# Kernel tuning notes

Hardware: AMD Instinct MI355X
Metric: run time of the kernel (lower is better)

The kernel has to match this reference:

```python
import jax, jax.numpy as jnp
import numpy as np

N = 50000   # nodes
E = 640000  # edges
IN = 256    # in_dim
H = 128     # hidden
OUT = 40    # out_dim
EPS = 1e-5  # BatchNorm eps


def setup_inputs() -> dict:
    key = jax.random.key(0)
    ks = jax.random.split(key, 14)
    x = jax.random.normal(ks[0], (N, IN), jnp.float32)
    edge_index = jax.random.randint(ks[1], (2, E), 0, N)
    def lin(k, fan_in, shape):
        return jax.random.normal(k, shape, jnp.float32) / np.float32(np.sqrt(fan_in))
    return {
        "x": x,
        "edge_index": edge_index,
        # block 0 (256 -> 128, has res_proj)
        "W0": lin(ks[2], IN, (IN, H)),
        "b0": jnp.zeros((H,), jnp.float32),
        "g0": jnp.ones((H,), jnp.float32),
        "be0": jnp.zeros((H,), jnp.float32),
        "pW": lin(ks[3], IN, (IN, H)),
        "pb": jnp.zeros((H,), jnp.float32),
        # block 1 (128 -> 128, identity residual)
        "W1": lin(ks[4], H, (H, H)),
        "b1": jnp.zeros((H,), jnp.float32),
        "g1": jnp.ones((H,), jnp.float32),
        "be1": jnp.zeros((H,), jnp.float32),
        # head
        "hW": lin(ks[5], H, (H, OUT)),
        "hb": jnp.zeros((OUT,), jnp.float32),
    }


def _gcn_conv(x, W, b, edge_index):
    """GCNConv(improved=True): x' = D^-1/2 (A + 2I) D^-1/2 (x W) + b."""
    h = x @ W  # [N, dout]
    row, col = edge_index[0], edge_index[1]  # source -> target
    # degree of A + 2I (edge_weight = 1, self-loop fill = 2.0)
    deg = jnp.zeros((N,), h.dtype).at[col].add(1.0) + 2.0
    dis = jax.lax.rsqrt(deg)  # deg > 0 always (self-loops)
    norm = dis[row] * dis[col]  # [E]
    # neighbor aggregation: scatter-add normalized messages to targets
    agg = jnp.zeros_like(h).at[col].add(norm[:, None] * h[row])
    # self-loop contribution with weight 2.0
    agg = agg + (2.0 * dis * dis)[:, None] * h
    return agg + b


def _bn(x, gamma, beta):
    # batch statistics (training-mode BatchNorm math), biased variance
    m = jnp.mean(x, axis=0)
    v = jnp.mean(jnp.square(x - m), axis=0)
    return (x - m) * jax.lax.rsqrt(v + EPS) * gamma + beta


def reference(x, edge_index, W0, b0, g0, be0, pW, pb, W1, b1, g1, be1, hW, hb):
    # block 0: conv -> bn -> relu -> (+ res_proj(x))
    out = jax.nn.relu(_bn(_gcn_conv(x, W0, b0, edge_index), g0, be0))
    x1 = out + (x @ pW + pb)
    # block 1: conv -> bn -> relu -> (+ identity)
    out = jax.nn.relu(_bn(_gcn_conv(x1, W1, b1, edge_index), g1, be1))
    x2 = out + x1
    return x2 @ hW + hb  # [N, OUT]
```

## Files before the change

kernel.cpp:

```cpp
#include <hip/hip_runtime.h>

#define H 128
#define IN_DIM 256
#define OUT_DIM 40
#define EPS 1e-5f

typedef unsigned short ushortT;
typedef __attribute__((ext_vector_type(8))) short bf16x8;
typedef __attribute__((ext_vector_type(4))) float f32x4;

static __device__ __forceinline__ ushortT f2bf(float f) {
    union { float f; unsigned u; } v; v.f = f;
    unsigned r = v.u + 0x7FFF + ((v.u >> 16) & 1);
    return (ushortT)(r >> 16);
}
static __device__ __forceinline__ unsigned pk2(float a, float b) {
    return (unsigned)f2bf(a) | ((unsigned)f2bf(b) << 16);
}
static __device__ __forceinline__ float bflo(unsigned v) {
    union { unsigned u; float f; } t; t.u = v << 16; return t.f;
}
static __device__ __forceinline__ float bfhi(unsigned v) {
    union { unsigned u; float f; } t; t.u = v & 0xFFFF0000u; return t.f;
}
static __device__ __forceinline__ float i2f(int v) {
    union { int i; float f; } t; t.i = v; return t.f;
}
static __device__ __forceinline__ int f2i(float v) {
    union { float f; int i; } t; t.f = v; return t.i;
}


__global__ __launch_bounds__(256) void count_xcd(const int* __restrict__ ei, int E, int nper,
                                                 int* __restrict__ cnt) {
    int xcd = blockIdx.x & 7;
    int nchunk = gridDim.x >> 3;
    int chunk = blockIdx.x >> 3;
    int csz = (E + nchunk - 1) / nchunk;
    int beg = chunk * csz;
    int end = min(E, beg + csz);
    for (int e = beg + (int)threadIdx.x; e < end; e += 256) {
        int c = ei[E + e];
        if (c / nper == xcd) atomicAdd(&cnt[c], 1);
    }
}

__global__ __launch_bounds__(256) void scan_block_sum(const int* __restrict__ cnt, int* __restrict__ bsum,
                                                      float* __restrict__ dis, int N) {
    __shared__ int s[256];
    int i = blockIdx.x * 256 + threadIdx.x;
    int c = (i < N) ? cnt[i] : -1;
    int v = (i < N) ? c + 1 : 0;
    if (i < N) dis[i] = rsqrtf((float)c + 2.0f);
    s[threadIdx.x] = v;
    __syncthreads();
    for (int o = 128; o > 0; o >>= 1) {
        if (threadIdx.x < o) s[threadIdx.x] += s[threadIdx.x + o];
        __syncthreads();
    }
    if (threadIdx.x == 0) bsum[blockIdx.x] = s[0];
}

__global__ void scan_tops(const int* __restrict__ bsum, int* __restrict__ boff, int* __restrict__ rowptrN, int nb) {
    __shared__ int s[256];
    int t = threadIdx.x;
    int v = (t < nb) ? bsum[t] : 0;
    s[t] = v;
    __syncthreads();
    for (int o = 1; o < 256; o <<= 1) {
        int u = (t >= o) ? s[t - o] : 0;
        __syncthreads();
        s[t] += u;
        __syncthreads();
    }
    if (t < nb) boff[t] = s[t] - v;
    if (t == 255) *rowptrN = s[255];
}

__global__ __launch_bounds__(256) void scan_final(const int* __restrict__ cnt, const int* __restrict__ boff,
                                                  const float* __restrict__ dis,
                                                  int* __restrict__ rowptr, int* __restrict__ cursor,
                                                  int2* __restrict__ recs, int N) {
    __shared__ int s[256];
    int t = threadIdx.x;
    int i = blockIdx.x * 256 + t;
    int v = (i < N) ? cnt[i] + 1 : 0;
    s[t] = v;
    __syncthreads();
    for (int o = 1; o < 256; o <<= 1) {
        int u = (t >= o) ? s[t - o] : 0;
        __syncthreads();
        s[t] += u;
        __syncthreads();
    }
    if (i < N) {
        int e = boff[blockIdx.x] + s[t] - v;
        rowptr[i] = e;
        cursor[i] = e + 1;
        float d = dis[i];
        int2 r; r.x = i; r.y = f2i(2.0f * d * d);
        recs[e] = r;
    }
}

__global__ __launch_bounds__(256) void fill_xcd(const int* __restrict__ ei, int E, int nper,
                                                const float* __restrict__ dis,
                                                int* __restrict__ cursor, int2* __restrict__ recs) {
    int xcd = blockIdx.x & 7;
    int nchunk = gridDim.x >> 3;
    int chunk = blockIdx.x >> 3;
    int csz = (E + nchunk - 1) / nchunk;
    int beg = chunk * csz;
    int end = min(E, beg + csz);
    for (int e = beg + (int)threadIdx.x; e < end; e += 256) {
        int c = ei[E + e];
        if (c / nper == xcd) {
            int r = ei[e];
            int slot = atomicAdd(&cursor[c], 1);
            int2 rec; rec.x = r; rec.y = f2i(dis[r] * dis[c]);
            recs[slot] = rec;
        }
    }
}


__global__ __launch_bounds__(256) void prep_weights(const float* __restrict__ W0, const float* __restrict__ pW,
                                                    const float* __restrict__ W1, const float* __restrict__ hW,
                                                    ushortT* __restrict__ Wt0, ushortT* __restrict__ WtP,
                                                    ushortT* __restrict__ Wt1, ushortT* __restrict__ WtH,
                                                    int* __restrict__ cnt, float* __restrict__ stats, int N) {
    int i = blockIdx.x * 256 + threadIdx.x;
    if (i < 32768) { int n = i >> 8, k = i & 255; Wt0[i] = f2bf(W0[k * 128 + n]); WtP[i] = f2bf(pW[k * 128 + n]); }
    if (i < 16384) { int n = i >> 7, k = i & 127; Wt1[i] = f2bf(W1[k * 128 + n]); }
    if (i < 6144)  { int n = i >> 7, k = i & 127; WtH[i] = (n < OUT_DIM) ? f2bf(hW[k * OUT_DIM + n]) : (ushortT)0; }
    if (i < N) cnt[i] = 0;
    if (i < 512) stats[i] = 0.f;
}


static __device__ __forceinline__ void g0_loads(const float* __restrict__ X, int brow, int kc,
                                                int tid, int N, float4 pf[4]) {
#pragma unroll
    for (int i = 0; i < 4; ++i) {
        int idx = i * 512 + tid;
        int row = idx >> 5, c4 = idx & 31;
        int gr = brow + row;
        pf[i] = make_float4(0.f, 0.f, 0.f, 0.f);
        if (gr < N) pf[i] = *(const float4*)&X[(size_t)gr * IN_DIM + kc * 128 + c4 * 4];
    }
}
static __device__ __forceinline__ void g0_write(ushortT* __restrict__ Sbuf, int tid, const float4 pf[4]) {
#pragma unroll
    for (int i = 0; i < 4; ++i) {
        int idx = i * 512 + tid;
        int row = idx >> 5, c4 = idx & 31;
        uint2 p;
        p.x = pk2(pf[i].x, pf[i].y);
        p.y = pk2(pf[i].z, pf[i].w);
        *(uint2*)&Sbuf[row * 136 + c4 * 4] = p;
    }
}

__global__ __launch_bounds__(512) void mgemm0d(const float* __restrict__ X,
                                               const ushortT* __restrict__ Wt0,
                                               const ushortT* __restrict__ WtP,
                                               const float* __restrict__ pb,
                                               ushortT* __restrict__ Oh,
                                               ushortT* __restrict__ Op,
                                               int N) {
    __shared__ __align__(16) ushortT S2[2][64 * 136];
    int tid = threadIdx.x;
    int brow = blockIdx.x * 64;
    int w = tid >> 6, lane = tid & 63;
    int lm = lane & 15, lk = lane >> 4;
    int mat = w >> 2;
    int colbase = (w & 3) * 32;
    const ushortT* Wt = mat ? WtP : Wt0;

    bf16x8 breg[2][8];
#pragma unroll
    for (int nt = 0; nt < 2; ++nt)
#pragma unroll
        for (int kk = 0; kk < 8; ++kk)
            breg[nt][kk] = *(const bf16x8*)&Wt[(size_t)(colbase + nt * 16 + lm) * IN_DIM + kk * 32 + lk * 8];
    float bb[2];
    bb[0] = mat ? pb[colbase + lm] : 0.f;
    bb[1] = mat ? pb[colbase + 16 + lm] : 0.f;

    float4 pf[4];
    g0_loads(X, brow, 0, tid, N, pf);
    g0_write(S2[0], tid, pf);
    __syncthreads();
    g0_loads(X, brow, 1, tid, N, pf);

    f32x4 acc[4][2];
#pragma unroll
    for (int mt = 0; mt < 4; ++mt)
#pragma unroll
        for (int nt = 0; nt < 2; ++nt) acc[mt][nt] = (f32x4)0.f;

#pragma unroll
    for (int kk = 0; kk < 4; ++kk) {
        bf16x8 af[4];
#pragma unroll
        for (int mt = 0; mt < 4; ++mt)
            af[mt] = *(const bf16x8*)&S2[0][(mt * 16 + lm) * 136 + kk * 32 + lk * 8];
#pragma unroll
        for (int nt = 0; nt < 2; ++nt)
#pragma unroll
            for (int mt = 0; mt < 4; ++mt)
                acc[mt][nt] = __builtin_amdgcn_mfma_f32_16x16x32_bf16(af[mt], breg[nt][kk], acc[mt][nt], 0, 0, 0);
    }
    g0_write(S2[1], tid, pf);
    __syncthreads();
#pragma unroll
    for (int kk = 0; kk < 4; ++kk) {
        bf16x8 af[4];
#pragma unroll
        for (int mt = 0; mt < 4; ++mt)
            af[mt] = *(const bf16x8*)&S2[1][(mt * 16 + lm) * 136 + kk * 32 + lk * 8];
#pragma unroll
        for (int nt = 0; nt < 2; ++nt)
#pragma unroll
            for (int mt = 0; mt < 4; ++mt)
                acc[mt][nt] = __builtin_amdgcn_mfma_f32_16x16x32_bf16(af[mt], breg[nt][4 + kk], acc[mt][nt], 0, 0, 0);
    }
    __syncthreads();
#pragma unroll
    for (int mt = 0; mt < 4; ++mt)
#pragma unroll
        for (int nt = 0; nt < 2; ++nt) {
            int col = colbase + nt * 16 + lm;
#pragma unroll
            for (int j = 0; j < 4; ++j) {
                int row = mt * 16 + lk * 4 + j;
                S2[mat][row * 136 + col] = f2bf(acc[mt][nt][j] + bb[nt]);
            }
        }
    __syncthreads();
#pragma unroll
    for (int i = 0; i < 4; ++i) {
        int idx = i * 512 + tid;
        int m2 = idx >> 10;
        int rem = idx & 1023;
        int row = rem >> 4, colq = rem & 15;
        int gr = brow + row;
        if (gr < N) {
            uint4 v = *(const uint4*)&S2[m2][row * 136 + colq * 8];
            ushortT* O = m2 ? Op : Oh;
            *(uint4*)&O[(size_t)gr * 128 + colq * 8] = v;
        }
    }
}


__global__ __launch_bounds__(512) void mgemm1_fused(const uint4* __restrict__ aggb,
                                                    const uint4* __restrict__ projb,
                                                    const float* __restrict__ stats,
                                                    const float* __restrict__ g,
                                                    const float* __restrict__ be,
                                                    const ushortT* __restrict__ Wt1,
                                                    ushortT* __restrict__ O,
                                                    uint4* __restrict__ x1b,
                                                    int N) {
    __shared__ __align__(16) ushortT S[17408];
    __shared__ float sc[128], sh[128];
    int tid = threadIdx.x;
    int brow = blockIdx.x * 128;

    if (tid < 128) {
        float mean = stats[tid] / (float)N;
        float var = stats[128 + tid] / (float)N - mean * mean;
        float inv = rsqrtf(var + EPS);
        float s = g[tid] * inv;
        sc[tid] = s;
        sh[tid] = be[tid] - mean * s;
    }
    __syncthreads();

#pragma unroll
    for (int i = 0; i < 4; ++i) {
        int idx = i * 512 + tid;
        int row = idx >> 4, q = idx & 15;
        int gr = brow + row;
        uint4 a = make_uint4(0u, 0u, 0u, 0u), p = a;
        if (gr < N) {
            size_t gidx = (size_t)gr * 16 + q;
            a = aggb[gidx];
            p = projb[gidx];
        }
        int ch = q * 8;
        float v0 = fmaxf(fmaf(bflo(a.x), sc[ch + 0], sh[ch + 0]), 0.f) + bflo(p.x);
        float v1 = fmaxf(fmaf(bfhi(a.x), sc[ch + 1], sh[ch + 1]), 0.f) + bfhi(p.x);
        float v2 = fmaxf(fmaf(bflo(a.y), sc[ch + 2], sh[ch + 2]), 0.f) + bflo(p.y);
        float v3 = fmaxf(fmaf(bfhi(a.y), sc[ch + 3], sh[ch + 3]), 0.f) + bfhi(p.y);
        float v4 = fmaxf(fmaf(bflo(a.z), sc[ch + 4], sh[ch + 4]), 0.f) + bflo(p.z);
        float v5 = fmaxf(fmaf(bfhi(a.z), sc[ch + 5], sh[ch + 5]), 0.f) + bfhi(p.z);
        float v6 = fmaxf(fmaf(bflo(a.w), sc[ch + 6], sh[ch + 6]), 0.f) + bflo(p.w);
        float v7 = fmaxf(fmaf(bfhi(a.w), sc[ch + 7], sh[ch + 7]), 0.f) + bfhi(p.w);
        uint4 pv;
        pv.x = pk2(v0, v1);
        pv.y = pk2(v2, v3);
        pv.z = pk2(v4, v5);
        pv.w = pk2(v6, v7);
        *(uint4*)&S[row * 136 + q * 8] = pv;
        if (gr < N) x1b[(size_t)gr * 16 + q] = pv;
    }
    __syncthreads();

    int w = tid >> 6, lane = tid & 63;
    int lm = lane & 15, lk = lane >> 4;
    int rh = (w >> 2) * 64;
    int colbase = (w & 3) * 32;

    bf16x8 breg[2][4];
#pragma unroll
    for (int nt = 0; nt < 2; ++nt)
#pragma unroll
        for (int ks = 0; ks < 4; ++ks)
            breg[nt][ks] = *(const bf16x8*)&Wt1[(size_t)(colbase + nt * 16 + lm) * H + ks * 32 + lk * 8];

    f32x4 acc[4][2];
#pragma unroll
    for (int mt = 0; mt < 4; ++mt)
#pragma unroll
        for (int nt = 0; nt < 2; ++nt) acc[mt][nt] = (f32x4)0.f;

#pragma unroll
    for (int ks = 0; ks < 4; ++ks) {
        bf16x8 af[4];
#pragma unroll
        for (int mt = 0; mt < 4; ++mt)
            af[mt] = *(const bf16x8*)&S[(rh + mt * 16 + lm) * 136 + ks * 32 + lk * 8];
#pragma unroll
        for (int nt = 0; nt < 2; ++nt)
#pragma unroll
            for (int mt = 0; mt < 4; ++mt)
                acc[mt][nt] = __builtin_amdgcn_mfma_f32_16x16x32_bf16(af[mt], breg[nt][ks], acc[mt][nt], 0, 0, 0);
    }

    __syncthreads();
#pragma unroll
    for (int mt = 0; mt < 4; ++mt)
#pragma unroll
        for (int nt = 0; nt < 2; ++nt) {
            int col = colbase + nt * 16 + lm;
#pragma unroll
            for (int j = 0; j < 4; ++j) {
                int row = rh + mt * 16 + lk * 4 + j;
                S[row * 136 + col] = f2bf(acc[mt][nt][j]);
            }
        }
    __syncthreads();
#pragma unroll
    for (int i = 0; i < 4; ++i) {
        int idx = i * 512 + tid;
        int row = idx >> 4, colq = idx & 15;
        int gr = brow + row;
        if (gr < N) {
            uint4 v = *(const uint4*)&S[row * 136 + colq * 8];
            *(uint4*)&O[(size_t)gr * 128 + colq * 8] = v;
        }
    }
}


__global__ __launch_bounds__(256) void aggregate_rec(const ushortT* __restrict__ h,
                                                     const int* __restrict__ rowptr,
                                                     const int2* __restrict__ recs,
                                                     ushortT* __restrict__ aggb, int N) {
    int n = blockIdx.x * 4 + (threadIdx.x >> 6);
    if (n >= N) return;
    int lane = threadIdx.x & 63;
    int half = lane >> 5, cl = lane & 31;
    int beg = rowptr[n], end = rowptr[n + 1];
    const uint2* h2 = (const uint2*)h;
    float a0 = 0.f, a1 = 0.f, a2 = 0.f, a3 = 0.f;
    float b0 = 0.f, b1 = 0.f, b2 = 0.f, b3 = 0.f;
    int idx = beg + half;
    for (; idx + 2 < end; idx += 4) {
        int2 r0 = recs[idx];
        int2 r1 = recs[idx + 2];
        uint2 v0 = h2[(size_t)r0.x * 32 + cl];
        uint2 v1 = h2[(size_t)r1.x * 32 + cl];
        float n0 = i2f(r0.y), n1 = i2f(r1.y);
        a0 = fmaf(n0, bflo(v0.x), a0); a1 = fmaf(n0, bfhi(v0.x), a1);
        a2 = fmaf(n0, bflo(v0.y), a2); a3 = fmaf(n0, bfhi(v0.y), a3);
        b0 = fmaf(n1, bflo(v1.x), b0); b1 = fmaf(n1, bfhi(v1.x), b1);
        b2 = fmaf(n1, bflo(v1.y), b2); b3 = fmaf(n1, bfhi(v1.y), b3);
    }
    if (idx < end) {
        int2 r0 = recs[idx];
        uint2 v0 = h2[(size_t)r0.x * 32 + cl];
        float n0 = i2f(r0.y);
        a0 = fmaf(n0, bflo(v0.x), a0); a1 = fmaf(n0, bfhi(v0.x), a1);
        a2 = fmaf(n0, bflo(v0.y), a2); a3 = fmaf(n0, bfhi(v0.y), a3);
    }
    a0 += b0; a1 += b1; a2 += b2; a3 += b3;
    a0 += __shfl_xor(a0, 32);
    a1 += __shfl_xor(a1, 32);
    a2 += __shfl_xor(a2, 32);
    a3 += __shfl_xor(a3, 32);
    if (half == 0) {
        uint2 o;
        o.x = pk2(a0, a1);
        o.y = pk2(a2, a3);
        ((uint2*)aggb)[(size_t)n * 32 + cl] = o;
    }
}


__global__ __launch_bounds__(256) void stats_bf(const unsigned* __restrict__ v, int totalU,
                                                float* __restrict__ sums) {
    int tid = blockIdx.x * 256 + threadIdx.x;
    int stride = gridDim.x * 256;
    float sx = 0.f, sy = 0.f, qx = 0.f, qy = 0.f;
    for (int i = tid; i < totalU; i += stride) {
        unsigned u = v[i];
        float a = bflo(u), b = bfhi(u);
        sx += a; sy += b;
        qx = fmaf(a, a, qx); qy = fmaf(b, b, qy);
    }
    __shared__ float l0[256], l1[256], l2[256], l3[256];
    int t = threadIdx.x;
    l0[t] = sx; l1[t] = sy; l2[t] = qx; l3[t] = qy;
    __syncthreads();
    if (t < 64) {
        sx = (l0[t] + l0[t + 64]) + (l0[t + 128] + l0[t + 192]);
        sy = (l1[t] + l1[t + 64]) + (l1[t + 128] + l1[t + 192]);
        qx = (l2[t] + l2[t + 64]) + (l2[t + 128] + l2[t + 192]);
        qy = (l3[t] + l3[t + 64]) + (l3[t + 128] + l3[t + 192]);
        atomicAdd(&sums[2 * t], sx);
        atomicAdd(&sums[2 * t + 1], sy);
        atomicAdd(&sums[128 + 2 * t], qx);
        atomicAdd(&sums[128 + 2 * t + 1], qy);
    }
}


__global__ __launch_bounds__(256) void head_fused(const uint4* __restrict__ aggb,
                                                  const uint4* __restrict__ x1b,
                                                  const float* __restrict__ stats,
                                                  const float* __restrict__ g,
                                                  const float* __restrict__ be,
                                                  const ushortT* __restrict__ WtH,
                                                  const float* __restrict__ hb,
                                                  float* __restrict__ out, int N) {
    __shared__ __align__(16) ushortT As[64][136];
    __shared__ __align__(16) ushortT Bs[48][136];
    __shared__ float sc[128], sh[128];

    int tid = threadIdx.x;
    int brow = blockIdx.x * 64;
    int w = tid >> 6, lane = tid & 63;
    int lm = lane & 15, lk = lane >> 4;

    if (tid < 128) {
        float mean = stats[tid] / (float)N;
        float var = stats[128 + tid] / (float)N - mean * mean;
        float inv = rsqrtf(var + EPS);
        float s = g[tid] * inv;
        sc[tid] = s;
        sh[tid] = be[tid] - mean * s;
    }
    if (tid < 192) {
        int row = tid >> 2, q = tid & 3;
        const uint4* src = (const uint4*)&WtH[(size_t)row * H + q * 32];
        uint4 a = src[0], b = src[1], c = src[2], d = src[3];
        uint4* dst = (uint4*)&Bs[row][q * 32];
        dst[0] = a; dst[1] = b; dst[2] = c; dst[3] = d;
    }
    __syncthreads();
#pragma unroll
    for (int k = 0; k < 4; ++k) {
        int idx = k * 256 + tid;
        int row = idx >> 4, colq = idx & 15;
        int gr = brow + row;
        uint4 a = make_uint4(0u, 0u, 0u, 0u), x = a;
        if (gr < N) {
            size_t gidx = (size_t)brow * 16 + idx;
            a = aggb[gidx];
            x = x1b[gidx];
        }
        int ch = colq * 8;
        float v0 = fmaxf(fmaf(bflo(a.x), sc[ch + 0], sh[ch + 0]), 0.f) + bflo(x.x);
        float v1 = fmaxf(fmaf(bfhi(a.x), sc[ch + 1], sh[ch + 1]), 0.f) + bfhi(x.x);
        float v2 = fmaxf(fmaf(bflo(a.y), sc[ch + 2], sh[ch + 2]), 0.f) + bflo(x.y);
        float v3 = fmaxf(fmaf(bfhi(a.y), sc[ch + 3], sh[ch + 3]), 0.f) + bfhi(x.y);
        float v4 = fmaxf(fmaf(bflo(a.z), sc[ch + 4], sh[ch + 4]), 0.f) + bflo(x.z);
        float v5 = fmaxf(fmaf(bfhi(a.z), sc[ch + 5], sh[ch + 5]), 0.f) + bfhi(x.z);
        float v6 = fmaxf(fmaf(bflo(a.w), sc[ch + 6], sh[ch + 6]), 0.f) + bflo(x.w);
        float v7 = fmaxf(fmaf(bfhi(a.w), sc[ch + 7], sh[ch + 7]), 0.f) + bfhi(x.w);
        uint4 pv;
        pv.x = pk2(v0, v1);
        pv.y = pk2(v2, v3);
        pv.z = pk2(v4, v5);
        pv.w = pk2(v6, v7);
        *(uint4*)&As[row][colq * 8] = pv;
    }
    __syncthreads();

    f32x4 acc[3];
#pragma unroll
    for (int nt = 0; nt < 3; ++nt) acc[nt] = (f32x4)0.f;
#pragma unroll
    for (int ks = 0; ks < 4; ++ks) {
        bf16x8 a = *(const bf16x8*)&As[w * 16 + lm][ks * 32 + lk * 8];
#pragma unroll
        for (int nt = 0; nt < 3; ++nt) {
            bf16x8 b = *(const bf16x8*)&Bs[nt * 16 + lm][ks * 32 + lk * 8];
            acc[nt] = __builtin_amdgcn_mfma_f32_16x16x32_bf16(a, b, acc[nt], 0, 0, 0);
        }
    }
#pragma unroll
    for (int nt = 0; nt < 3; ++nt) {
        int col = nt * 16 + lm;
        if (col < OUT_DIM) {
            float bbv = hb[col];
#pragma unroll
            for (int j = 0; j < 4; ++j) {
                int r = brow + w * 16 + lk * 4 + j;
                if (r < N) out[(size_t)r * OUT_DIM + col] = acc[nt][j] + bbv;
            }
        }
    }
}


extern "C" void kernel_launch(void* const* d_in, const int* in_sizes, int n_in,
                              void* d_out, int out_size, void* d_ws, size_t ws_size,
                              hipStream_t stream) {
    const float* x   = (const float*)d_in[0];
    const int*   ei  = (const int*)d_in[1];
    const float* W0  = (const float*)d_in[2];
    const float* g0  = (const float*)d_in[4];
    const float* be0 = (const float*)d_in[5];
    const float* pW  = (const float*)d_in[6];
    const float* pb  = (const float*)d_in[7];
    const float* W1  = (const float*)d_in[8];
    const float* g1  = (const float*)d_in[10];
    const float* be1 = (const float*)d_in[11];
    const float* hW  = (const float*)d_in[12];
    const float* hb  = (const float*)d_in[13];
    float* out = (float*)d_out;

    int N = in_sizes[0] / IN_DIM;
    int E = in_sizes[1] / 2;
    size_t NH = (size_t)N * H;

    ushortT* hb16   = (ushortT*)d_ws;
    ushortT* aggb   = hb16 + NH;
    ushortT* projb  = aggb + NH;
    ushortT* x1b    = projb + NH;
    float*   dis    = (float*)(x1b + NH);
    int*     cnt    = (int*)(dis + N);
    int*     rowptr = cnt + N;
    int*     cursor = rowptr + (N + 1);
    int2*    recs   = (int2*)(cursor + N);
    float*   stats  = (float*)(recs + (E + N));
    ushortT* Wt0    = (ushortT*)(stats + 512);
    ushortT* WtP    = Wt0 + 128 * 256;
    ushortT* Wt1    = WtP + 128 * 256;
    ushortT* WtH    = Wt1 + 128 * 128;
    int*     bsum   = (int*)(WtH + 48 * 128);
    int*     boff   = bsum + 256;
    float*   stats0 = stats;
    float*   stats1 = stats + 256;

    int nb = (N + 255) / 256;
    int g64 = (N + 63) / 64;
    int g128 = (N + 127) / 128;
    int gAgg = (N + 3) / 4;

    prep_weights<<<196, 256, 0, stream>>>(W0, pW, W1, hW, Wt0, WtP, Wt1, WtH, cnt, stats, N);
    count_xcd<<<2048, 256, 0, stream>>>(ei, E, (N + 7) / 8, cnt);
    scan_block_sum<<<nb, 256, 0, stream>>>(cnt, bsum, dis, N);
    scan_tops<<<1, 256, 0, stream>>>(bsum, boff, &rowptr[N], nb);
    scan_final<<<nb, 256, 0, stream>>>(cnt, boff, dis, rowptr, cursor, recs, N);
    fill_xcd<<<2048, 256, 0, stream>>>(ei, E, (N + 7) / 8, dis, cursor, recs);

    mgemm0d<<<g64, 512, 0, stream>>>(x, Wt0, WtP, pb, hb16, projb, N);
    aggregate_rec<<<gAgg, 256, 0, stream>>>(hb16, rowptr, recs, aggb, N);
    stats_bf<<<256, 256, 0, stream>>>((const unsigned*)aggb, (int)(NH / 2), stats0);

    mgemm1_fused<<<g128, 512, 0, stream>>>((const uint4*)aggb, (const uint4*)projb, stats0, g0, be0,
                                           Wt1, hb16, (uint4*)x1b, N);
    aggregate_rec<<<gAgg, 256, 0, stream>>>(hb16, rowptr, recs, aggb, N);
    stats_bf<<<256, 256, 0, stream>>>((const unsigned*)aggb, (int)(NH / 2), stats1);

    head_fused<<<g64, 256, 0, stream>>>((const uint4*)aggb, (const uint4*)x1b, stats1, g1, be1,
                                        WtH, hb, out, N);
}
```

Measured before the change: 251.7 us.

## Fuse degree counting into first GEMM launch and unroll aggregation by four

The degree-count kernel is merged into the first GEMM launch as extra blocks after the GEMM blocks, so the edge counting runs alongside the independent X·W0/X·pW GEMM instead of as a separate serialized launch. The GEMM is moved ahead of the CSR scan and fill steps. The aggregate kernel now handles four edges per half-wave per iteration with four accumulator sets instead of two, giving more memory-level parallelism on the gathers. The cost is more registers in aggregation, and count blocks that share the 512-thread launch configuration and LDS allocation with the GEMM blocks.

```diff
diff --git a/kernel.cpp b/kernel.cpp
--- a/kernel.cpp
+++ b/kernel.cpp
@@ -31,19 +31,153 @@
 }
 
 
-__global__ __launch_bounds__(256) void count_xcd(const int* __restrict__ ei, int E, int nper,
-                                                 int* __restrict__ cnt) {
-    int xcd = blockIdx.x & 7;
-    int nchunk = gridDim.x >> 3;
-    int chunk = blockIdx.x >> 3;
-    int csz = (E + nchunk - 1) / nchunk;
-    int beg = chunk * csz;
-    int end = min(E, beg + csz);
-    for (int e = beg + (int)threadIdx.x; e < end; e += 256) {
-        int c = ei[E + e];
-        if (c / nper == xcd) atomicAdd(&cnt[c], 1);
-    }
-}
+__global__ __launch_bounds__(256) void prep_weights(const float* __restrict__ W0, const float* __restrict__ pW,
+                                                    const float* __restrict__ W1, const float* __restrict__ hW,
+                                                    ushortT* __restrict__ Wt0, ushortT* __restrict__ WtP,
+                                                    ushortT* __restrict__ Wt1, ushortT* __restrict__ WtH,
+                                                    int* __restrict__ cnt, float* __restrict__ stats, int N) {
+    int i = blockIdx.x * 256 + threadIdx.x;
+    if (i < 32768) { int n = i >> 8, k = i & 255; Wt0[i] = f2bf(W0[k * 128 + n]); WtP[i] = f2bf(pW[k * 128 + n]); }
+    if (i < 16384) { int n = i >> 7, k = i & 127; Wt1[i] = f2bf(W1[k * 128 + n]); }
+    if (i < 6144)  { int n = i >> 7, k = i & 127; WtH[i] = (n < OUT_DIM) ? f2bf(hW[k * OUT_DIM + n]) : (ushortT)0; }
+    if (i < N) cnt[i] = 0;
+    if (i < 512) stats[i] = 0.f;
+}
+
+
+static __device__ __forceinline__ void g0_loads(const float* __restrict__ X, int brow, int kc,
+                                                int tid, int N, float4 pf[4]) {
+#pragma unroll
+    for (int i = 0; i < 4; ++i) {
+        int idx = i * 512 + tid;
+        int row = idx >> 5, c4 = idx & 31;
+        int gr = brow + row;
+        pf[i] = make_float4(0.f, 0.f, 0.f, 0.f);
+        if (gr < N) pf[i] = *(const float4*)&X[(size_t)gr * IN_DIM + kc * 128 + c4 * 4];
+    }
+}
+static __device__ __forceinline__ void g0_write(ushortT* __restrict__ Sbuf, int tid, const float4 pf[4]) {
+#pragma unroll
+    for (int i = 0; i < 4; ++i) {
+        int idx = i * 512 + tid;
+        int row = idx >> 5, c4 = idx & 31;
+        uint2 p;
+        p.x = pk2(pf[i].x, pf[i].y);
+        p.y = pk2(pf[i].z, pf[i].w);
+        *(uint2*)&Sbuf[row * 136 + c4 * 4] = p;
+    }
+}
+
+__global__ __launch_bounds__(512) void gemm0_count(const float* __restrict__ X,
+                                                   const ushortT* __restrict__ Wt0,
+                                                   const ushortT* __restrict__ WtP,
+                                                   const float* __restrict__ pb,
+                                                   ushortT* __restrict__ Oh,
+                                                   ushortT* __restrict__ Op,
+                                                   const int* __restrict__ ei,
+                                                   int* __restrict__ cnt,
+                                                   int N, int E, int nper, int gemmBlocks) {
+    __shared__ __align__(16) ushortT S2[2][64 * 136];
+    int tid = threadIdx.x;
+
+    if (blockIdx.x >= gemmBlocks) {
+        int cbid = blockIdx.x - gemmBlocks;
+        int xcd = cbid & 7;
+        int nchunk = (gridDim.x - gemmBlocks) >> 3;
+        int chunk = cbid >> 3;
+        int csz = (E + nchunk - 1) / nchunk;
+        int beg = chunk * csz;
+        int end = min(E, beg + csz);
+        for (int e = beg + tid; e < end; e += 512) {
+            int c = ei[E + e];
+            if (c / nper == xcd) atomicAdd(&cnt[c], 1);
+        }
+        return;
+    }
+
+    int brow = blockIdx.x * 64;
+    int w = tid >> 6, lane = tid & 63;
+    int lm = lane & 15, lk = lane >> 4;
+    int mat = w >> 2;
+    int colbase = (w & 3) * 32;
+    const ushortT* Wt = mat ? WtP : Wt0;
+
+    bf16x8 breg[2][8];
+#pragma unroll
+    for (int nt = 0; nt < 2; ++nt)
+#pragma unroll
+        for (int kk = 0; kk < 8; ++kk)
+            breg[nt][kk] = *(const bf16x8*)&Wt[(size_t)(colbase + nt * 16 + lm) * IN_DIM + kk * 32 + lk * 8];
+    float bb[2];
+    bb[0] = mat ? pb[colbase + lm] : 0.f;
+    bb[1] = mat ? pb[colbase + 16 + lm] : 0.f;
+
+    float4 pf[4];
+    g0_loads(X, brow, 0, tid, N, pf);
+    g0_write(S2[0], tid, pf);
+    __syncthreads();
+    g0_loads(X, brow, 1, tid, N, pf);
+
+    f32x4 acc[4][2];
+#pragma unroll
+    for (int mt = 0; mt < 4; ++mt)
+#pragma unroll
+        for (int nt = 0; nt < 2; ++nt) acc[mt][nt] = (f32x4)0.f;
+
+#pragma unroll
+    for (int kk = 0; kk < 4; ++kk) {
+        bf16x8 af[4];
+#pragma unroll
+        for (int mt = 0; mt < 4; ++mt)
+            af[mt] = *(const bf16x8*)&S2[0][(mt * 16 + lm) * 136 + kk * 32 + lk * 8];
+#pragma unroll
+        for (int nt = 0; nt < 2; ++nt)
+#pragma unroll
+            for (int mt = 0; mt < 4; ++mt)
+                acc[mt][nt] = __builtin_amdgcn_mfma_f32_16x16x32_bf16(af[mt], breg[nt][kk], acc[mt][nt], 0, 0, 0);
+    }
+    g0_write(S2[1], tid, pf);
+    __syncthreads();
+#pragma unroll
+    for (int kk = 0; kk < 4; ++kk) {
+        bf16x8 af[4];
+#pragma unroll
+        for (int mt = 0; mt < 4; ++mt)
+            af[mt] = *(const bf16x8*)&S2[1][(mt * 16 + lm) * 136 + kk * 32 + lk * 8];
+#pragma unroll
+        for (int nt = 0; nt < 2; ++nt)
+#pragma unroll
+            for (int mt = 0; mt < 4; ++mt)
+                acc[mt][nt] = __builtin_amdgcn_mfma_f32_16x16x32_bf16(af[mt], breg[nt][4 + kk], acc[mt][nt], 0, 0, 0);
+    }
+    __syncthreads();
+#pragma unroll
+    for (int mt = 0; mt < 4; ++mt)
+#pragma unroll
+        for (int nt = 0; nt < 2; ++nt) {
+            int col = colbase + nt * 16 + lm;
+#pragma unroll
+            for (int j = 0; j < 4; ++j) {
+                int row = mt * 16 + lk * 4 + j;
+                S2[mat][row * 136 + col] = f2bf(acc[mt][nt][j] + bb[nt]);
+            }
+        }
+    __syncthreads();
+#pragma unroll
+    for (int i = 0; i < 4; ++i) {
+        int idx = i * 512 + tid;
+        int m2 = idx >> 10;
+        int rem = idx & 1023;
+        int row = rem >> 4, colq = rem & 15;
+        int gr = brow + row;
+        if (gr < N) {
+            uint4 v = *(const uint4*)&S2[m2][row * 136 + colq * 8];
+            ushortT* O = m2 ? Op : Oh;
+            *(uint4*)&O[(size_t)gr * 128 + colq * 8] = v;
+        }
+    }
+}
+
 
 __global__ __launch_bounds__(256) void scan_block_sum(const int* __restrict__ cnt, int* __restrict__ bsum,
                                                       float* __restrict__ dis, int N) {
@@ -124,132 +258,88 @@
 }
 
 
-__global__ __launch_bounds__(256) void prep_weights(const float* __restrict__ W0, const float* __restrict__ pW,
-                                                    const float* __restrict__ W1, const float* __restrict__ hW,
-                                                    ushortT* __restrict__ Wt0, ushortT* __restrict__ WtP,
-                                                    ushortT* __restrict__ Wt1, ushortT* __restrict__ WtH,
-                                                    int* __restrict__ cnt, float* __restrict__ stats, int N) {
-    int i = blockIdx.x * 256 + threadIdx.x;
-    if (i < 32768) { int n = i >> 8, k = i & 255; Wt0[i] = f2bf(W0[k * 128 + n]); WtP[i] = f2bf(pW[k * 128 + n]); }
-    if (i < 16384) { int n = i >> 7, k = i & 127; Wt1[i] = f2bf(W1[k * 128 + n]); }
-    if (i < 6144)  { int n = i >> 7, k = i & 127; WtH[i] = (n < OUT_DIM) ? f2bf(hW[k * OUT_DIM + n]) : (ushortT)0; }
-    if (i < N) cnt[i] = 0;
-    if (i < 512) stats[i] = 0.f;
-}
-
-
-static __device__ __forceinline__ void g0_loads(const float* __restrict__ X, int brow, int kc,
-                                                int tid, int N, float4 pf[4]) {
-#pragma unroll
-    for (int i = 0; i < 4; ++i) {
-        int idx = i * 512 + tid;
-        int row = idx >> 5, c4 = idx & 31;
-        int gr = brow + row;
-        pf[i] = make_float4(0.f, 0.f, 0.f, 0.f);
-        if (gr < N) pf[i] = *(const float4*)&X[(size_t)gr * IN_DIM + kc * 128 + c4 * 4];
-    }
-}
-static __device__ __forceinline__ void g0_write(ushortT* __restrict__ Sbuf, int tid, const float4 pf[4]) {
-#pragma unroll
-    for (int i = 0; i < 4; ++i) {
-        int idx = i * 512 + tid;
-        int row = idx >> 5, c4 = idx & 31;
-        uint2 p;
-        p.x = pk2(pf[i].x, pf[i].y);
-        p.y = pk2(pf[i].z, pf[i].w);
-        *(uint2*)&Sbuf[row * 136 + c4 * 4] = p;
-    }
-}
-
-__global__ __launch_bounds__(512) void mgemm0d(const float* __restrict__ X,
-                                               const ushortT* __restrict__ Wt0,
-                                               const ushortT* __restrict__ WtP,
-                                               const float* __restrict__ pb,
-                                               ushortT* __restrict__ Oh,
-                                               ushortT* __restrict__ Op,
-                                               int N) {
-    __shared__ __align__(16) ushortT S2[2][64 * 136];
-    int tid = threadIdx.x;
-    int brow = blockIdx.x * 64;
-    int w = tid >> 6, lane = tid & 63;
-    int lm = lane & 15, lk = lane >> 4;
-    int mat = w >> 2;
-    int colbase = (w & 3) * 32;
-    const ushortT* Wt = mat ? WtP : Wt0;
-
-    bf16x8 breg[2][8];
-#pragma unroll
-    for (int nt = 0; nt < 2; ++nt)
-#pragma unroll
-        for (int kk = 0; kk < 8; ++kk)
-            breg[nt][kk] = *(const bf16x8*)&Wt[(size_t)(colbase + nt * 16 + lm) * IN_DIM + kk * 32 + lk * 8];
-    float bb[2];
-    bb[0] = mat ? pb[colbase + lm] : 0.f;
-    bb[1] = mat ? pb[colbase + 16 + lm] : 0.f;
-
-    float4 pf[4];
-    g0_loads(X, brow, 0, tid, N, pf);
-    g0_write(S2[0], tid, pf);
-    __syncthreads();
-    g0_loads(X, brow, 1, tid, N, pf);
-
-    f32x4 acc[4][2];
-#pragma unroll
-    for (int mt = 0; mt < 4; ++mt)
-#pragma unroll
-        for (int nt = 0; nt < 2; ++nt) acc[mt][nt] = (f32x4)0.f;
-
-#pragma unroll
-    for (int kk = 0; kk < 4; ++kk) {
-        bf16x8 af[4];
-#pragma unroll
-        for (int mt = 0; mt < 4; ++mt)
-            af[mt] = *(const bf16x8*)&S2[0][(mt * 16 + lm) * 136 + kk * 32 + lk * 8];
-#pragma unroll
-        for (int nt = 0; nt < 2; ++nt)
-#pragma unroll
-            for (int mt = 0; mt < 4; ++mt)
-                acc[mt][nt] = __builtin_amdgcn_mfma_f32_16x16x32_bf16(af[mt], breg[nt][kk], acc[mt][nt], 0, 0, 0);
-    }
-    g0_write(S2[1], tid, pf);
-    __syncthreads();
-#pragma unroll
-    for (int kk = 0; kk < 4; ++kk) {
-        bf16x8 af[4];
-#pragma unroll
-        for (int mt = 0; mt < 4; ++mt)
-            af[mt] = *(const bf16x8*)&S2[1][(mt * 16 + lm) * 136 + kk * 32 + lk * 8];
-#pragma unroll
-        for (int nt = 0; nt < 2; ++nt)
-#pragma unroll
-            for (int mt = 0; mt < 4; ++mt)
-                acc[mt][nt] = __builtin_amdgcn_mfma_f32_16x16x32_bf16(af[mt], breg[nt][4 + kk], acc[mt][nt], 0, 0, 0);
-    }
-    __syncthreads();
-#pragma unroll
-    for (int mt = 0; mt < 4; ++mt)
-#pragma unroll
-        for (int nt = 0; nt < 2; ++nt) {
-            int col = colbase + nt * 16 + lm;
-#pragma unroll
-            for (int j = 0; j < 4; ++j) {
-                int row = mt * 16 + lk * 4 + j;
-                S2[mat][row * 136 + col] = f2bf(acc[mt][nt][j] + bb[nt]);
-            }
-        }
-    __syncthreads();
-#pragma unroll
-    for (int i = 0; i < 4; ++i) {
-        int idx = i * 512 + tid;
-        int m2 = idx >> 10;
-        int rem = idx & 1023;
-        int row = rem >> 4, colq = rem & 15;
-        int gr = brow + row;
-        if (gr < N) {
-            uint4 v = *(const uint4*)&S2[m2][row * 136 + colq * 8];
-            ushortT* O = m2 ? Op : Oh;
-            *(uint4*)&O[(size_t)gr * 128 + colq * 8] = v;
-        }
+__global__ __launch_bounds__(256) void aggregate_rec(const ushortT* __restrict__ h,
+                                                     const int* __restrict__ rowptr,
+                                                     const int2* __restrict__ recs,
+                                                     ushortT* __restrict__ aggb, int N) {
+    int n = blockIdx.x * 4 + (threadIdx.x >> 6);
+    if (n >= N) return;
+    int lane = threadIdx.x & 63;
+    int half = lane >> 5, cl = lane & 31;
+    int beg = rowptr[n], end = rowptr[n + 1];
+    const uint2* h2 = (const uint2*)h;
+    float a0 = 0.f, a1 = 0.f, a2 = 0.f, a3 = 0.f;
+    float b0 = 0.f, b1 = 0.f, b2 = 0.f, b3 = 0.f;
+    float c0 = 0.f, c1 = 0.f, c2 = 0.f, c3 = 0.f;
+    float d0 = 0.f, d1 = 0.f, d2 = 0.f, d3 = 0.f;
+    int idx = beg + half;
+    for (; idx + 6 < end; idx += 8) {
+        int2 r0 = recs[idx];
+        int2 r1 = recs[idx + 2];
+        int2 r2 = recs[idx + 4];
+        int2 r3 = recs[idx + 6];
+        uint2 v0 = h2[(size_t)r0.x * 32 + cl];
+        uint2 v1 = h2[(size_t)r1.x * 32 + cl];
+        uint2 v2 = h2[(size_t)r2.x * 32 + cl];
+        uint2 v3 = h2[(size_t)r3.x * 32 + cl];
+        float n0 = i2f(r0.y), n1 = i2f(r1.y), n2 = i2f(r2.y), n3 = i2f(r3.y);
+        a0 = fmaf(n0, bflo(v0.x), a0); a1 = fmaf(n0, bfhi(v0.x), a1);
+        a2 = fmaf(n0, bflo(v0.y), a2); a3 = fmaf(n0, bfhi(v0.y), a3);
+        b0 = fmaf(n1, bflo(v1.x), b0); b1 = fmaf(n1, bfhi(v1.x), b1);
+        b2 = fmaf(n1, bflo(v1.y), b2); b3 = fmaf(n1, bfhi(v1.y), b3);
+        c0 = fmaf(n2, bflo(v2.x), c0); c1 = fmaf(n2, bfhi(v2.x), c1);
+        c2 = fmaf(n2, bflo(v2.y), c2); c3 = fmaf(n2, bfhi(v2.y), c3);
+        d0 = fmaf(n3, bflo(v3.x), d0); d1 = fmaf(n3, bfhi(v3.x), d1);
+        d2 = fmaf(n3, bflo(v3.y), d2); d3 = fmaf(n3, bfhi(v3.y), d3);
+    }
+    for (; idx < end; idx += 2) {
+        int2 r0 = recs[idx];
+        uint2 v0 = h2[(size_t)r0.x * 32 + cl];
+        float n0 = i2f(r0.y);
+        a0 = fmaf(n0, bflo(v0.x), a0); a1 = fmaf(n0, bfhi(v0.x), a1);
+        a2 = fmaf(n0, bflo(v0.y), a2); a3 = fmaf(n0, bfhi(v0.y), a3);
+    }
+    a0 = (a0 + b0) + (c0 + d0);
+    a1 = (a1 + b1) + (c1 + d1);
+    a2 = (a2 + b2) + (c2 + d2);
+    a3 = (a3 + b3) + (c3 + d3);
+    a0 += __shfl_xor(a0, 32);
+    a1 += __shfl_xor(a1, 32);
+    a2 += __shfl_xor(a2, 32);
+    a3 += __shfl_xor(a3, 32);
+    if (half == 0) {
+        uint2 o;
+        o.x = pk2(a0, a1);
+        o.y = pk2(a2, a3);
+        ((uint2*)aggb)[(size_t)n * 32 + cl] = o;
+    }
+}
+
+
+__global__ __launch_bounds__(256) void stats_bf(const unsigned* __restrict__ v, int totalU,
+                                                float* __restrict__ sums) {
+    int tid = blockIdx.x * 256 + threadIdx.x;
+    int stride = gridDim.x * 256;
+    float sx = 0.f, sy = 0.f, qx = 0.f, qy = 0.f;
+    for (int i = tid; i < totalU; i += stride) {
+        unsigned u = v[i];
+        float a = bflo(u), b = bfhi(u);
+        sx += a; sy += b;
+        qx = fmaf(a, a, qx); qy = fmaf(b, b, qy);
+    }
+    __shared__ float l0[256], l1[256], l2[256], l3[256];
+    int t = threadIdx.x;
+    l0[t] = sx; l1[t] = sy; l2[t] = qx; l3[t] = qy;
+    __syncthreads();
+    if (t < 64) {
+        sx = (l0[t] + l0[t + 64]) + (l0[t + 128] + l0[t + 192]);
+        sy = (l1[t] + l1[t + 64]) + (l1[t + 128] + l1[t + 192]);
+        qx = (l2[t] + l2[t + 64]) + (l2[t + 128] + l2[t + 192]);
+        qy = (l3[t] + l3[t + 64]) + (l3[t + 128] + l3[t + 192]);
+        atomicAdd(&sums[2 * t], sx);
+        atomicAdd(&sums[2 * t + 1], sy);
+        atomicAdd(&sums[128 + 2 * t], qx);
+        atomicAdd(&sums[128 + 2 * t + 1], qy);
     }
 }
 
@@ -361,79 +451,6 @@
             uint4 v = *(const uint4*)&S[row * 136 + colq * 8];
             *(uint4*)&O[(size_t)gr * 128 + colq * 8] = v;
         }
-    }
-}
-
-
-__global__ __launch_bounds__(256) void aggregate_rec(const ushortT* __restrict__ h,
-                                                     const int* __restrict__ rowptr,
-                                                     const int2* __restrict__ recs,
-                                                     ushortT* __restrict__ aggb, int N) {
-    int n = blockIdx.x * 4 + (threadIdx.x >> 6);
-    if (n >= N) return;
-    int lane = threadIdx.x & 63;
-    int half = lane >> 5, cl = lane & 31;
-    int beg = rowptr[n], end = rowptr[n + 1];
-    const uint2* h2 = (const uint2*)h;
-    float a0 = 0.f, a1 = 0.f, a2 = 0.f, a3 = 0.f;
-    float b0 = 0.f, b1 = 0.f, b2 = 0.f, b3 = 0.f;
-    int idx = beg + half;
-    for (; idx + 2 < end; idx += 4) {
-        int2 r0 = recs[idx];
-        int2 r1 = recs[idx + 2];
-        uint2 v0 = h2[(size_t)r0.x * 32 + cl];
-        uint2 v1 = h2[(size_t)r1.x * 32 + cl];
-        float n0 = i2f(r0.y), n1 = i2f(r1.y);
-        a0 = fmaf(n0, bflo(v0.x), a0); a1 = fmaf(n0, bfhi(v0.x), a1);
-        a2 = fmaf(n0, bflo(v0.y), a2); a3 = fmaf(n0, bfhi(v0.y), a3);
-        b0 = fmaf(n1, bflo(v1.x), b0); b1 = fmaf(n1, bfhi(v1.x), b1);
-        b2 = fmaf(n1, bflo(v1.y), b2); b3 = fmaf(n1, bfhi(v1.y), b3);
-    }
-    if (idx < end) {
-        int2 r0 = recs[idx];
-        uint2 v0 = h2[(size_t)r0.x * 32 + cl];
-        float n0 = i2f(r0.y);
-        a0 = fmaf(n0, bflo(v0.x), a0); a1 = fmaf(n0, bfhi(v0.x), a1);
-        a2 = fmaf(n0, bflo(v0.y), a2); a3 = fmaf(n0, bfhi(v0.y), a3);
-    }
-    a0 += b0; a1 += b1; a2 += b2; a3 += b3;
-    a0 += __shfl_xor(a0, 32);
-    a1 += __shfl_xor(a1, 32);
-    a2 += __shfl_xor(a2, 32);
-    a3 += __shfl_xor(a3, 32);
-    if (half == 0) {
-        uint2 o;
-        o.x = pk2(a0, a1);
-        o.y = pk2(a2, a3);
-        ((uint2*)aggb)[(size_t)n * 32 + cl] = o;
-    }
-}
-
-
-__global__ __launch_bounds__(256) void stats_bf(const unsigned* __restrict__ v, int totalU,
-                                                float* __restrict__ sums) {
-    int tid = blockIdx.x * 256 + threadIdx.x;
-    int stride = gridDim.x * 256;
-    float sx = 0.f, sy = 0.f, qx = 0.f, qy = 0.f;
-    for (int i = tid; i < totalU; i += stride) {
-        unsigned u = v[i];
-        float a = bflo(u), b = bfhi(u);
-        sx += a; sy += b;
-        qx = fmaf(a, a, qx); qy = fmaf(b, b, qy);
-    }
-    __shared__ float l0[256], l1[256], l2[256], l3[256];
-    int t = threadIdx.x;
-    l0[t] = sx; l1[t] = sy; l2[t] = qx; l3[t] = qy;
-    __syncthreads();
-    if (t < 64) {
-        sx = (l0[t] + l0[t + 64]) + (l0[t + 128] + l0[t + 192]);
-        sy = (l1[t] + l1[t + 64]) + (l1[t + 128] + l1[t + 192]);
-        qx = (l2[t] + l2[t + 64]) + (l2[t + 128] + l2[t + 192]);
-        qy = (l3[t] + l3[t + 64]) + (l3[t + 128] + l3[t + 192]);
-        atomicAdd(&sums[2 * t], sx);
-        atomicAdd(&sums[2 * t + 1], sy);
-        atomicAdd(&sums[128 + 2 * t], qx);
-        atomicAdd(&sums[128 + 2 * t + 1], qy);
     }
 }
 
@@ -571,15 +588,19 @@
     int g64 = (N + 63) / 64;
     int g128 = (N + 127) / 128;
     int gAgg = (N + 3) / 4;
+    int nper = (N + 7) / 8;
+    const int CNT_BLOCKS = 1024;
 
     prep_weights<<<196, 256, 0, stream>>>(W0, pW, W1, hW, Wt0, WtP, Wt1, WtH, cnt, stats, N);
-    count_xcd<<<2048, 256, 0, stream>>>(ei, E, (N + 7) / 8, cnt);
+
+    gemm0_count<<<g64 + CNT_BLOCKS, 512, 0, stream>>>(x, Wt0, WtP, pb, hb16, projb,
+                                                      ei, cnt, N, E, nper, g64);
+
     scan_block_sum<<<nb, 256, 0, stream>>>(cnt, bsum, dis, N);
     scan_tops<<<1, 256, 0, stream>>>(bsum, boff, &rowptr[N], nb);
     scan_final<<<nb, 256, 0, stream>>>(cnt, boff, dis, rowptr, cursor, recs, N);
-    fill_xcd<<<2048, 256, 0, stream>>>(ei, E, (N + 7) / 8, dis, cursor, recs);
-
-    mgemm0d<<<g64, 512, 0, stream>>>(x, Wt0, WtP, pb, hb16, projb, N);
+    fill_xcd<<<2048, 256, 0, stream>>>(ei, E, nper, dis, cursor, recs);
+
     aggregate_rec<<<gAgg, 256, 0, stream>>>(hb16, rowptr, recs, aggb, N);
     stats_bf<<<256, 256, 0, stream>>>((const unsigned*)aggb, (int)(NH / 2), stats0);
 
```

Result: faster. 244.7 us (-2.8%).
